# Optimization experiments

Measured on AMD Instinct MI355X. Metric: run time of the kernel, lower is better.

The kernel has to match this reference:

```python
import jax, jax.numpy as jnp
import numpy as np

IN, OUT, RANK = 4096, 4096, 8
ALPHA = 8.0

def _quantize_int8(x):
    # row-wise symmetric int8 quantization (matches torch _quantize_int8)
    scale = jnp.max(jnp.abs(x), axis=1) / 127.0              # [rows]
    q = jnp.round(x / jnp.clip(scale, 1e-12)[:, None]).astype(jnp.int8)
    return q, scale


def setup_inputs() -> dict:
    key = jax.random.key(0)
    k_x, k_w, k_a, k_b = jax.random.split(key, 4)
    x = jax.random.normal(k_x, (8192, IN), dtype=jnp.float32)
    # simulate quantizing a pretrained fp32 weight [OUT, IN]
    w = jax.random.normal(k_w, (OUT, IN), dtype=jnp.float32) * 0.02
    w_scale = jnp.max(jnp.abs(w), axis=1) / 127.0
    weight_i8 = jnp.round(w / jnp.clip(w_scale, 1e-12)[:, None]).astype(jnp.int8)
    weight_scale = w_scale.astype(jnp.float32)               # [OUT]
    # LoRA params (lora_b random instead of zeros so output is nontrivial)
    lora_a = jax.random.normal(k_a, (RANK, IN), dtype=jnp.float32) * (1.0 / np.sqrt(IN))
    lora_b = jax.random.normal(k_b, (OUT, RANK), dtype=jnp.float32) * 0.02
    return {"x": x, "weight_i8": weight_i8, "weight_scale": weight_scale,
            "lora_a": lora_a, "lora_b": lora_b}


def reference(x, weight_i8, weight_scale, lora_a, lora_b):
    # quantize_act=True path: int8 activation quant + int8 GEMM (int32 accum) + dequant
    x_i8, x_scale = _quantize_int8(x)                         # [T, IN] int8, [T]
    out_i32 = jnp.matmul(x_i8, weight_i8.T, preferred_element_type=jnp.int32)  # [T, OUT]
    out = out_i32.astype(jnp.float32) * x_scale[:, None] * weight_scale[None, :]
    # LoRA low-rank add: x @ A^T @ B^T * (alpha / rank)
    out = out + (x @ lora_a.T) @ lora_b.T * (ALPHA / RANK)
    return out
```

## Files before the change

kernel.cpp:

```cpp
#include <hip/hip_runtime.h>
#include <stdint.h>

#define T_DIM   8192
#define IN_DIM  4096
#define OUT_DIM 4096
#define RANK    8

typedef int v4i __attribute__((ext_vector_type(4)));

__device__ __forceinline__ void async_copy16(const void* g, void* l) {
  __builtin_amdgcn_global_load_lds(
      (const __attribute__((address_space(1))) void*)g,
      (__attribute__((address_space(3))) void*)l, 16, 0, 0);
}

#define PW_BLOCKS 16384
#define QX_BLOCKS 8192
#define LA_BLOCKS 16
#define XZ_BLOCKS 64
#define PREP_BLOCKS (PW_BLOCKS + QX_BLOCKS + LA_BLOCKS + XZ_BLOCKS)

__global__ __launch_bounds__(256) void prep(
    const int* __restrict__ w32,
    const float* __restrict__ x,
    const float* __restrict__ lora_a,
    int8_t* __restrict__ w8,
    int8_t* __restrict__ x_i8,
    float* __restrict__ x_scale,
    int8_t* __restrict__ a_i8,
    float* __restrict__ a_scale,
    float* __restrict__ xa)
{
  const int b = blockIdx.x;
  const int tid = threadIdx.x;
  __shared__ float red[4];

  if (b < PW_BLOCKS) {
    const int idx = b * 256 + tid;
    const int4 v = ((const int4*)w32)[idx];
    char4 q;
    q.x = (signed char)v.x; q.y = (signed char)v.y;
    q.z = (signed char)v.z; q.w = (signed char)v.w;
    ((char4*)w8)[idx] = q;
    return;
  }
  if (b < PW_BLOCKS + QX_BLOCKS) {
    const int row = b - PW_BLOCKS;
    const float4* xr = (const float4*)(x + (size_t)row * IN_DIM);
    float4 xv[4];
#pragma unroll
    for (int c = 0; c < 4; ++c) xv[c] = xr[c * 256 + tid];
    float am = 0.f;
#pragma unroll
    for (int c = 0; c < 4; ++c)
      am = fmaxf(am, fmaxf(fmaxf(fabsf(xv[c].x), fabsf(xv[c].y)),
                           fmaxf(fabsf(xv[c].z), fabsf(xv[c].w))));
#pragma unroll
    for (int off = 32; off > 0; off >>= 1)
      am = fmaxf(am, __shfl_xor(am, off, 64));
    if ((tid & 63) == 0) red[tid >> 6] = am;
    __syncthreads();
    const float amax = fmaxf(fmaxf(red[0], red[1]), fmaxf(red[2], red[3]));
    const float scale = amax * (1.0f / 127.0f);
    const float inv = 1.0f / fmaxf(scale, 1e-12f);
    char4* qout = (char4*)(x_i8 + (size_t)row * IN_DIM);
#pragma unroll
    for (int c = 0; c < 4; ++c) {
      char4 q;
      q.x = (signed char)(int)rintf(xv[c].x * inv);
      q.y = (signed char)(int)rintf(xv[c].y * inv);
      q.z = (signed char)(int)rintf(xv[c].z * inv);
      q.w = (signed char)(int)rintf(xv[c].w * inv);
      qout[c * 256 + tid] = q;
    }
    if (tid == 0) x_scale[row] = scale;
    return;
  }
  if (b < PW_BLOCKS + QX_BLOCKS + LA_BLOCKS) {
    const int r = b - (PW_BLOCKS + QX_BLOCKS);
    if (r >= RANK) {
      ((int4*)(a_i8 + (size_t)r * IN_DIM))[tid] = int4{0, 0, 0, 0};
      if (tid == 0) a_scale[r] = 0.f;
      return;
    }
    const float4* ar = (const float4*)(lora_a + (size_t)r * IN_DIM);
    float4 av[4];
#pragma unroll
    for (int c = 0; c < 4; ++c) av[c] = ar[c * 256 + tid];
    float am = 0.f;
#pragma unroll
    for (int c = 0; c < 4; ++c)
      am = fmaxf(am, fmaxf(fmaxf(fabsf(av[c].x), fabsf(av[c].y)),
                           fmaxf(fabsf(av[c].z), fabsf(av[c].w))));
#pragma unroll
    for (int off = 32; off > 0; off >>= 1)
      am = fmaxf(am, __shfl_xor(am, off, 64));
    if ((tid & 63) == 0) red[tid >> 6] = am;
    __syncthreads();
    const float amax = fmaxf(fmaxf(red[0], red[1]), fmaxf(red[2], red[3]));
    const float scale = amax * (1.0f / 127.0f);
    const float inv = 1.0f / fmaxf(scale, 1e-12f);
    char4* qout = (char4*)(a_i8 + (size_t)r * IN_DIM);
#pragma unroll
    for (int c = 0; c < 4; ++c) {
      char4 q;
      q.x = (signed char)(int)rintf(av[c].x * inv);
      q.y = (signed char)(int)rintf(av[c].y * inv);
      q.z = (signed char)(int)rintf(av[c].z * inv);
      q.w = (signed char)(int)rintf(av[c].w * inv);
      qout[c * 256 + tid] = q;
    }
    if (tid == 0) a_scale[r] = scale;
    return;
  }
  const int idx = (b - (PW_BLOCKS + QX_BLOCKS + LA_BLOCKS)) * 256 + tid;
  ((float4*)xa)[idx] = float4{0.f, 0.f, 0.f, 0.f};
}

__global__ __launch_bounds__(256) void xa_i8(
    const int8_t* __restrict__ x_i8, const float* __restrict__ x_scale,
    const int8_t* __restrict__ a_i8, const float* __restrict__ a_scale,
    float* __restrict__ xa)
{
  const int tid = threadIdx.x;
  const int lane = tid & 63, wave = tid >> 6;
  const int kb = blockIdx.x & 7;
  const int rb = blockIdx.x >> 3;
  const int m16 = lane & 15, quad = lane >> 4;
  const int row0 = rb * 64 + wave * 16;
  const int kbase = kb * 512;

  v4i acc = {0, 0, 0, 0};
  const int8_t* ap = x_i8 + (size_t)(row0 + m16) * IN_DIM + kbase + quad * 16;
  const int8_t* bp = a_i8 + (size_t)m16 * IN_DIM + kbase + quad * 16;
#pragma unroll
  for (int k = 0; k < 512; k += 64)
    acc = __builtin_amdgcn_mfma_i32_16x16x64_i8(
        *(const v4i*)(ap + k), *(const v4i*)(bp + k), acc, 0, 0, 0);

  if (m16 < RANK) {
    const float asc = a_scale[m16];
    const int r = row0 + quad * 4;
#pragma unroll
    for (int reg = 0; reg < 4; ++reg)
      atomicAdd(&xa[(size_t)(r + reg) * RANK + m16],
                (float)acc[reg] * x_scale[r + reg] * asc);
  }
}

__global__ __launch_bounds__(256) void int8_gemm_lora(
    const int8_t* __restrict__ A,
    const int8_t* __restrict__ B,
    const float* __restrict__ x_scale,
    const float* __restrict__ w_scale,
    const float* __restrict__ xa,
    const float* __restrict__ lora_b,
    float* __restrict__ out)
{
  __shared__ __align__(16) int8_t As[128 * 64];
  __shared__ __align__(16) int8_t Bs[128 * 64];
  __shared__ float xs_s[128];
  __shared__ float ws_s[128];
  __shared__ __align__(16) float xa_s[128 * RANK];
  __shared__ __align__(16) float lb_s[128 * RANK];

  const int tid = threadIdx.x;
  const int bx = blockIdx.x & 31;
  const int by = blockIdx.x >> 5;
  const size_t arow0 = (size_t)by * 128;
  const size_t brow0 = (size_t)bx * 128;

  if (tid < 128) xs_s[tid] = x_scale[arow0 + tid];
  else           ws_s[tid - 128] = w_scale[brow0 + (tid - 128)];
  ((float4*)xa_s)[tid] = ((const float4*)(xa + arow0 * RANK))[tid];
  ((float4*)lb_s)[tid] = ((const float4*)(lora_b + brow0 * RANK))[tid];

  v4i acc[4][4];
  const v4i vzero = {0, 0, 0, 0};
#pragma unroll
  for (int i = 0; i < 4; ++i)
#pragma unroll
    for (int j = 0; j < 4; ++j) acc[i][j] = vzero;

  const int lane = tid & 63;
  const int wave = tid >> 6;
  const int wr = wave >> 1, wc = wave & 1;
  const int quad = lane >> 4, m16 = lane & 15;

  const int8_t* a_frag_base = As + ((wr * 64 + m16) * 64 + quad * 16);
  const int8_t* b_frag_base = Bs + ((wc * 64 + m16) * 64 + quad * 16);

  const int off0 = tid * 16;
  const int r0 = tid >> 2;
  const int c0 = (tid & 3) * 16;
  const int8_t* a_src = A + (arow0 + (size_t)r0) * IN_DIM + c0;
  const int8_t* b_src = B + (brow0 + (size_t)r0) * IN_DIM + c0;

  for (int k0 = 0; k0 < IN_DIM; k0 += 64) {
    async_copy16(a_src + k0,                       As + off0);
    async_copy16(a_src + (size_t)64 * IN_DIM + k0, As + 4096 + off0);
    async_copy16(b_src + k0,                       Bs + off0);
    async_copy16(b_src + (size_t)64 * IN_DIM + k0, Bs + 4096 + off0);
    __syncthreads();

    v4i aF[4], bF[4];
#pragma unroll
    for (int i = 0; i < 4; ++i) aF[i] = *(const v4i*)(a_frag_base + i * 16 * 64);
#pragma unroll
    for (int j = 0; j < 4; ++j) bF[j] = *(const v4i*)(b_frag_base + j * 16 * 64);
#pragma unroll
    for (int i = 0; i < 4; ++i)
#pragma unroll
      for (int j = 0; j < 4; ++j)
        acc[i][j] = __builtin_amdgcn_mfma_i32_16x16x64_i8(aF[i], bF[j], acc[i][j], 0, 0, 0);
    __syncthreads();
  }

  float wscv[4];
  float4 lb0[4], lb1[4];
  int cols[4];
#pragma unroll
  for (int j = 0; j < 4; ++j) {
    const int c = wc * 64 + j * 16 + m16;
    cols[j] = c;
    wscv[j] = ws_s[c];
    lb0[j] = *(const float4*)(lb_s + c * RANK);
    lb1[j] = *(const float4*)(lb_s + c * RANK + 4);
  }
#pragma unroll
  for (int i = 0; i < 4; ++i) {
#pragma unroll
    for (int reg = 0; reg < 4; ++reg) {
      const int r = wr * 64 + i * 16 + quad * 4 + reg;
      const float xsc = xs_s[r];
      const float4 xa0 = *(const float4*)(xa_s + r * RANK);
      const float4 xa1 = *(const float4*)(xa_s + r * RANK + 4);
      float* orow = out + (arow0 + (size_t)r) * OUT_DIM + brow0;
#pragma unroll
      for (int j = 0; j < 4; ++j) {
        float v = (float)acc[i][j][reg] * xsc * wscv[j];
        v += xa0.x * lb0[j].x + xa0.y * lb0[j].y + xa0.z * lb0[j].z + xa0.w * lb0[j].w +
             xa1.x * lb1[j].x + xa1.y * lb1[j].y + xa1.z * lb1[j].z + xa1.w * lb1[j].w;
        orow[cols[j]] = v;
      }
    }
  }
}

extern "C" void kernel_launch(void* const* d_in, const int* in_sizes, int n_in,
                              void* d_out, int out_size, void* d_ws, size_t ws_size,
                              hipStream_t stream) {
  const float* x       = (const float*)d_in[0];
  const int*   w_i32   = (const int*)d_in[1];
  const float* w_scale = (const float*)d_in[2];
  const float* lora_a  = (const float*)d_in[3];
  const float* lora_b  = (const float*)d_in[4];
  float* out = (float*)d_out;

  int8_t* x_i8   = (int8_t*)d_ws;
  int8_t* w8     = x_i8 + (size_t)T_DIM * IN_DIM;
  int8_t* a_i8   = w8 + (size_t)OUT_DIM * IN_DIM;
  float*  a_scale = (float*)(a_i8 + (size_t)16 * IN_DIM);
  float*  x_scale = a_scale + 16;
  float*  xa      = x_scale + T_DIM;

  prep<<<PREP_BLOCKS, 256, 0, stream>>>(w_i32, x, lora_a, w8, x_i8, x_scale,
                                        a_i8, a_scale, xa);
  xa_i8<<<(T_DIM / 64) * 8, 256, 0, stream>>>(x_i8, x_scale, a_i8, a_scale, xa);
  int8_gemm_lora<<<(T_DIM / 128) * (OUT_DIM / 128), 256, 0, stream>>>(
      x_i8, w8, x_scale, w_scale, xa, lora_b, out);
}
```

Before: 451.9 us.

## Fuse LoRA x@A into quant prep and use 256x256 triple-buffered int8 GEMM

The LoRA x@A^T product is now computed in fp32 inside the activation-quantization blocks, reusing the loaded x row. This removes the separate lora_a quantization, the xa zeroing, the MFMA xa kernel and its atomics. The main GEMM moves to 256x256 tiles with 512 threads and a three-stage global_load_lds pipeline. It adds an XOR-swizzled LDS layout, a remapped block order for L2 locality, and setprio around the MFMAs. The larger tile raises register pressure (8x4 accumulators) and uses 96KB of LDS, which limits occupancy.

```diff
diff --git a/kernel.cpp b/kernel.cpp
--- a/kernel.cpp
+++ b/kernel.cpp
@@ -16,9 +16,7 @@
 
 #define PW_BLOCKS 16384
 #define QX_BLOCKS 8192
-#define LA_BLOCKS 16
-#define XZ_BLOCKS 64
-#define PREP_BLOCKS (PW_BLOCKS + QX_BLOCKS + LA_BLOCKS + XZ_BLOCKS)
+#define PREP_BLOCKS (PW_BLOCKS + QX_BLOCKS)
 
 __global__ __launch_bounds__(256) void prep(
     const int* __restrict__ w32,
@@ -27,13 +25,12 @@
     int8_t* __restrict__ w8,
     int8_t* __restrict__ x_i8,
     float* __restrict__ x_scale,
-    int8_t* __restrict__ a_i8,
-    float* __restrict__ a_scale,
     float* __restrict__ xa)
 {
   const int b = blockIdx.x;
   const int tid = threadIdx.x;
   __shared__ float red[4];
+  __shared__ float redx[4][RANK];
 
   if (b < PW_BLOCKS) {
     const int idx = b * 256 + tid;
@@ -44,111 +41,99 @@
     ((char4*)w8)[idx] = q;
     return;
   }
-  if (b < PW_BLOCKS + QX_BLOCKS) {
-    const int row = b - PW_BLOCKS;
-    const float4* xr = (const float4*)(x + (size_t)row * IN_DIM);
-    float4 xv[4];
-#pragma unroll
-    for (int c = 0; c < 4; ++c) xv[c] = xr[c * 256 + tid];
-    float am = 0.f;
-#pragma unroll
-    for (int c = 0; c < 4; ++c)
-      am = fmaxf(am, fmaxf(fmaxf(fabsf(xv[c].x), fabsf(xv[c].y)),
-                           fmaxf(fabsf(xv[c].z), fabsf(xv[c].w))));
-#pragma unroll
-    for (int off = 32; off > 0; off >>= 1)
-      am = fmaxf(am, __shfl_xor(am, off, 64));
-    if ((tid & 63) == 0) red[tid >> 6] = am;
-    __syncthreads();
-    const float amax = fmaxf(fmaxf(red[0], red[1]), fmaxf(red[2], red[3]));
-    const float scale = amax * (1.0f / 127.0f);
-    const float inv = 1.0f / fmaxf(scale, 1e-12f);
-    char4* qout = (char4*)(x_i8 + (size_t)row * IN_DIM);
+
+  const int row = b - PW_BLOCKS;
+  const float4* xr = (const float4*)(x + (size_t)row * IN_DIM);
+  float4 xv[4];
+#pragma unroll
+  for (int c = 0; c < 4; ++c) xv[c] = xr[c * 256 + tid];
+
+  float am = 0.f;
+#pragma unroll
+  for (int c = 0; c < 4; ++c)
+    am = fmaxf(am, fmaxf(fmaxf(fabsf(xv[c].x), fabsf(xv[c].y)),
+                         fmaxf(fabsf(xv[c].z), fabsf(xv[c].w))));
+#pragma unroll
+  for (int off = 32; off > 0; off >>= 1)
+    am = fmaxf(am, __shfl_xor(am, off, 64));
+  if ((tid & 63) == 0) red[tid >> 6] = am;
+
+  float dot[RANK];
+#pragma unroll
+  for (int r = 0; r < RANK; ++r) {
+    const float4* ar = (const float4*)(lora_a + (size_t)r * IN_DIM);
+    float s = 0.f;
 #pragma unroll
     for (int c = 0; c < 4; ++c) {
-      char4 q;
-      q.x = (signed char)(int)rintf(xv[c].x * inv);
-      q.y = (signed char)(int)rintf(xv[c].y * inv);
-      q.z = (signed char)(int)rintf(xv[c].z * inv);
-      q.w = (signed char)(int)rintf(xv[c].w * inv);
-      qout[c * 256 + tid] = q;
+      const float4 a = ar[c * 256 + tid];
+      s += xv[c].x * a.x + xv[c].y * a.y + xv[c].z * a.z + xv[c].w * a.w;
     }
-    if (tid == 0) x_scale[row] = scale;
-    return;
-  }
-  if (b < PW_BLOCKS + QX_BLOCKS + LA_BLOCKS) {
-    const int r = b - (PW_BLOCKS + QX_BLOCKS);
-    if (r >= RANK) {
-      ((int4*)(a_i8 + (size_t)r * IN_DIM))[tid] = int4{0, 0, 0, 0};
-      if (tid == 0) a_scale[r] = 0.f;
-      return;
-    }
-    const float4* ar = (const float4*)(lora_a + (size_t)r * IN_DIM);
-    float4 av[4];
-#pragma unroll
-    for (int c = 0; c < 4; ++c) av[c] = ar[c * 256 + tid];
-    float am = 0.f;
-#pragma unroll
-    for (int c = 0; c < 4; ++c)
-      am = fmaxf(am, fmaxf(fmaxf(fabsf(av[c].x), fabsf(av[c].y)),
-                           fmaxf(fabsf(av[c].z), fabsf(av[c].w))));
-#pragma unroll
-    for (int off = 32; off > 0; off >>= 1)
-      am = fmaxf(am, __shfl_xor(am, off, 64));
-    if ((tid & 63) == 0) red[tid >> 6] = am;
-    __syncthreads();
-    const float amax = fmaxf(fmaxf(red[0], red[1]), fmaxf(red[2], red[3]));
-    const float scale = amax * (1.0f / 127.0f);
-    const float inv = 1.0f / fmaxf(scale, 1e-12f);
-    char4* qout = (char4*)(a_i8 + (size_t)r * IN_DIM);
-#pragma unroll
-    for (int c = 0; c < 4; ++c) {
-      char4 q;
-      q.x = (signed char)(int)rintf(av[c].x * inv);
-      q.y = (signed char)(int)rintf(av[c].y * inv);
-      q.z = (signed char)(int)rintf(av[c].z * inv);
-      q.w = (signed char)(int)rintf(av[c].w * inv);
-      qout[c * 256 + tid] = q;
-    }
-    if (tid == 0) a_scale[r] = scale;
-    return;
-  }
-  const int idx = (b - (PW_BLOCKS + QX_BLOCKS + LA_BLOCKS)) * 256 + tid;
-  ((float4*)xa)[idx] = float4{0.f, 0.f, 0.f, 0.f};
-}
-
-__global__ __launch_bounds__(256) void xa_i8(
-    const int8_t* __restrict__ x_i8, const float* __restrict__ x_scale,
-    const int8_t* __restrict__ a_i8, const float* __restrict__ a_scale,
-    float* __restrict__ xa)
-{
-  const int tid = threadIdx.x;
-  const int lane = tid & 63, wave = tid >> 6;
-  const int kb = blockIdx.x & 7;
-  const int rb = blockIdx.x >> 3;
-  const int m16 = lane & 15, quad = lane >> 4;
-  const int row0 = rb * 64 + wave * 16;
-  const int kbase = kb * 512;
-
-  v4i acc = {0, 0, 0, 0};
-  const int8_t* ap = x_i8 + (size_t)(row0 + m16) * IN_DIM + kbase + quad * 16;
-  const int8_t* bp = a_i8 + (size_t)m16 * IN_DIM + kbase + quad * 16;
-#pragma unroll
-  for (int k = 0; k < 512; k += 64)
-    acc = __builtin_amdgcn_mfma_i32_16x16x64_i8(
-        *(const v4i*)(ap + k), *(const v4i*)(bp + k), acc, 0, 0, 0);
-
-  if (m16 < RANK) {
-    const float asc = a_scale[m16];
-    const int r = row0 + quad * 4;
-#pragma unroll
-    for (int reg = 0; reg < 4; ++reg)
-      atomicAdd(&xa[(size_t)(r + reg) * RANK + m16],
-                (float)acc[reg] * x_scale[r + reg] * asc);
-  }
-}
-
-__global__ __launch_bounds__(256) void int8_gemm_lora(
+    dot[r] = s;
+  }
+#pragma unroll
+  for (int off = 32; off > 0; off >>= 1) {
+#pragma unroll
+    for (int r = 0; r < RANK; ++r)
+      dot[r] += __shfl_xor(dot[r], off, 64);
+  }
+  if ((tid & 63) == 0) {
+#pragma unroll
+    for (int r = 0; r < RANK; ++r) redx[tid >> 6][r] = dot[r];
+  }
+  __syncthreads();
+
+  const float amax = fmaxf(fmaxf(red[0], red[1]), fmaxf(red[2], red[3]));
+  const float scale = amax * (1.0f / 127.0f);
+  const float inv = 1.0f / fmaxf(scale, 1e-12f);
+  char4* qout = (char4*)(x_i8 + (size_t)row * IN_DIM);
+#pragma unroll
+  for (int c = 0; c < 4; ++c) {
+    char4 q;
+    q.x = (signed char)(int)rintf(xv[c].x * inv);
+    q.y = (signed char)(int)rintf(xv[c].y * inv);
+    q.z = (signed char)(int)rintf(xv[c].z * inv);
+    q.w = (signed char)(int)rintf(xv[c].w * inv);
+    qout[c * 256 + tid] = q;
+  }
+  if (tid == 0) x_scale[row] = scale;
+  if (tid < RANK)
+    xa[(size_t)row * RANK + tid] =
+        redx[0][tid] + redx[1][tid] + redx[2][tid] + redx[3][tid];
+}
+
+#define SYNC(n) do {                                      \
+    asm volatile("s_waitcnt vmcnt(" #n ")" ::: "memory"); \
+    __builtin_amdgcn_s_barrier();                         \
+    __builtin_amdgcn_sched_barrier(0);                    \
+  } while (0)
+
+__device__ __forceinline__ void stage_tile(const int8_t* aSrc, const int8_t* bSrc,
+                                           int8_t* Lbuf, int ldsOff) {
+  async_copy16(aSrc,                          Lbuf + ldsOff);
+  async_copy16(aSrc + (size_t)128 * IN_DIM,   Lbuf + 8192 + ldsOff);
+  async_copy16(bSrc,                          Lbuf + 16384 + ldsOff);
+  async_copy16(bSrc + (size_t)128 * IN_DIM,   Lbuf + 16384 + 8192 + ldsOff);
+}
+
+__device__ __forceinline__ void compute_tile(const int8_t* Lbuf, int aOff, int bOff,
+                                             v4i (&acc)[8][4]) {
+  const int8_t* La = Lbuf;
+  const int8_t* Lb = Lbuf + 16384;
+  v4i aF[8], bF[4];
+#pragma unroll
+  for (int i = 0; i < 8; ++i) aF[i] = *(const v4i*)(La + aOff + i * 1024);
+#pragma unroll
+  for (int j = 0; j < 4; ++j) bF[j] = *(const v4i*)(Lb + bOff + j * 1024);
+  __builtin_amdgcn_s_setprio(1);
+#pragma unroll
+  for (int i = 0; i < 8; ++i)
+#pragma unroll
+    for (int j = 0; j < 4; ++j)
+      acc[i][j] = __builtin_amdgcn_mfma_i32_16x16x64_i8(aF[i], bF[j], acc[i][j], 0, 0, 0);
+  __builtin_amdgcn_s_setprio(0);
+}
+
+__global__ __launch_bounds__(512, 2) void gemm256_i8(
     const int8_t* __restrict__ A,
     const int8_t* __restrict__ B,
     const float* __restrict__ x_scale,
@@ -157,64 +142,76 @@
     const float* __restrict__ lora_b,
     float* __restrict__ out)
 {
-  __shared__ __align__(16) int8_t As[128 * 64];
-  __shared__ __align__(16) int8_t Bs[128 * 64];
-  __shared__ float xs_s[128];
-  __shared__ float ws_s[128];
-  __shared__ __align__(16) float xa_s[128 * RANK];
-  __shared__ __align__(16) float lb_s[128 * RANK];
-
+  __shared__ __align__(16) int8_t smem[3 * 32768];
   const int tid = threadIdx.x;
-  const int bx = blockIdx.x & 31;
-  const int by = blockIdx.x >> 5;
-  const size_t arow0 = (size_t)by * 128;
-  const size_t brow0 = (size_t)bx * 128;
-
-  if (tid < 128) xs_s[tid] = x_scale[arow0 + tid];
-  else           ws_s[tid - 128] = w_scale[brow0 + (tid - 128)];
+
+  const int orig = blockIdx.x;
+  const int wgid = ((orig & 7) << 6) | (orig >> 3);
+  const int by = wgid >> 4;
+  const int bx = wgid & 15;
+  const size_t arow0 = (size_t)by * 256;
+  const size_t brow0 = (size_t)bx * 256;
+
+  const int r_l = tid >> 2;
+  const int qsw = ((tid & 3) ^ ((r_l >> 1) & 3)) << 4;
+  const int8_t* aSrc = A + (arow0 + r_l) * IN_DIM + qsw;
+  const int8_t* bSrc = B + (brow0 + r_l) * IN_DIM + qsw;
+  const int ldsOff = tid << 4;
+
+  const int lane = tid & 63;
+  const int wave = tid >> 6;
+  const int wr = wave >> 2, wc = wave & 3;
+  const int m16 = lane & 15, quad = lane >> 4;
+  const int sw = (quad ^ ((m16 >> 1) & 3)) << 4;
+  const int aOff = (wr * 128 + m16) * 64 + sw;
+  const int bOff = (wc * 64 + m16) * 64 + sw;
+
+  v4i acc[8][4];
+  const v4i vz = {0, 0, 0, 0};
+#pragma unroll
+  for (int i = 0; i < 8; ++i)
+#pragma unroll
+    for (int j = 0; j < 4; ++j) acc[i][j] = vz;
+
+  stage_tile(aSrc, bSrc, smem, ldsOff);
+  stage_tile(aSrc + 64, bSrc + 64, smem + 32768, ldsOff);
+
+#pragma unroll 1
+  for (int t = 0; t < 60; t += 3) {
+    SYNC(4);
+    stage_tile(aSrc + (t + 2) * 64, bSrc + (t + 2) * 64, smem + 2 * 32768, ldsOff);
+    compute_tile(smem, aOff, bOff, acc);
+    SYNC(4);
+    stage_tile(aSrc + (t + 3) * 64, bSrc + (t + 3) * 64, smem, ldsOff);
+    compute_tile(smem + 32768, aOff, bOff, acc);
+    SYNC(4);
+    stage_tile(aSrc + (t + 4) * 64, bSrc + (t + 4) * 64, smem + 32768, ldsOff);
+    compute_tile(smem + 2 * 32768, aOff, bOff, acc);
+  }
+  SYNC(4);
+  stage_tile(aSrc + 62 * 64, bSrc + 62 * 64, smem + 2 * 32768, ldsOff);
+  compute_tile(smem, aOff, bOff, acc);
+  SYNC(4);
+  stage_tile(aSrc + 63 * 64, bSrc + 63 * 64, smem, ldsOff);
+  compute_tile(smem + 32768, aOff, bOff, acc);
+  SYNC(4);
+  compute_tile(smem + 2 * 32768, aOff, bOff, acc);
+  asm volatile("s_waitcnt vmcnt(0)" ::: "memory");
+  __builtin_amdgcn_s_barrier();
+  __builtin_amdgcn_sched_barrier(0);
+  compute_tile(smem, aOff, bOff, acc);
+
+  __syncthreads();
+  float* fs   = (float*)smem;
+  float* xs_s = fs;
+  float* ws_s = fs + 256;
+  float* xa_s = fs + 512;
+  float* lb_s = fs + 2560;
+  if (tid < 256) xs_s[tid] = x_scale[arow0 + tid];
+  else           ws_s[tid - 256] = w_scale[brow0 + (tid - 256)];
   ((float4*)xa_s)[tid] = ((const float4*)(xa + arow0 * RANK))[tid];
   ((float4*)lb_s)[tid] = ((const float4*)(lora_b + brow0 * RANK))[tid];
-
-  v4i acc[4][4];
-  const v4i vzero = {0, 0, 0, 0};
-#pragma unroll
-  for (int i = 0; i < 4; ++i)
-#pragma unroll
-    for (int j = 0; j < 4; ++j) acc[i][j] = vzero;
-
-  const int lane = tid & 63;
-  const int wave = tid >> 6;
-  const int wr = wave >> 1, wc = wave & 1;
-  const int quad = lane >> 4, m16 = lane & 15;
-
-  const int8_t* a_frag_base = As + ((wr * 64 + m16) * 64 + quad * 16);
-  const int8_t* b_frag_base = Bs + ((wc * 64 + m16) * 64 + quad * 16);
-
-  const int off0 = tid * 16;
-  const int r0 = tid >> 2;
-  const int c0 = (tid & 3) * 16;
-  const int8_t* a_src = A + (arow0 + (size_t)r0) * IN_DIM + c0;
-  const int8_t* b_src = B + (brow0 + (size_t)r0) * IN_DIM + c0;
-
-  for (int k0 = 0; k0 < IN_DIM; k0 += 64) {
-    async_copy16(a_src + k0,                       As + off0);
-    async_copy16(a_src + (size_t)64 * IN_DIM + k0, As + 4096 + off0);
-    async_copy16(b_src + k0,                       Bs + off0);
-    async_copy16(b_src + (size_t)64 * IN_DIM + k0, Bs + 4096 + off0);
-    __syncthreads();
-
-    v4i aF[4], bF[4];
-#pragma unroll
-    for (int i = 0; i < 4; ++i) aF[i] = *(const v4i*)(a_frag_base + i * 16 * 64);
-#pragma unroll
-    for (int j = 0; j < 4; ++j) bF[j] = *(const v4i*)(b_frag_base + j * 16 * 64);
-#pragma unroll
-    for (int i = 0; i < 4; ++i)
-#pragma unroll
-      for (int j = 0; j < 4; ++j)
-        acc[i][j] = __builtin_amdgcn_mfma_i32_16x16x64_i8(aF[i], bF[j], acc[i][j], 0, 0, 0);
-    __syncthreads();
-  }
+  __syncthreads();
 
   float wscv[4];
   float4 lb0[4], lb1[4];
@@ -228,10 +225,10 @@
     lb1[j] = *(const float4*)(lb_s + c * RANK + 4);
   }
 #pragma unroll
-  for (int i = 0; i < 4; ++i) {
+  for (int i = 0; i < 8; ++i) {
 #pragma unroll
     for (int reg = 0; reg < 4; ++reg) {
-      const int r = wr * 64 + i * 16 + quad * 4 + reg;
+      const int r = wr * 128 + i * 16 + quad * 4 + reg;
       const float xsc = xs_s[r];
       const float4 xa0 = *(const float4*)(xa_s + r * RANK);
       const float4 xa1 = *(const float4*)(xa_s + r * RANK + 4);
@@ -257,16 +254,12 @@
   const float* lora_b  = (const float*)d_in[4];
   float* out = (float*)d_out;
 
-  int8_t* x_i8   = (int8_t*)d_ws;
-  int8_t* w8     = x_i8 + (size_t)T_DIM * IN_DIM;
-  int8_t* a_i8   = w8 + (size_t)OUT_DIM * IN_DIM;
-  float*  a_scale = (float*)(a_i8 + (size_t)16 * IN_DIM);
-  float*  x_scale = a_scale + 16;
+  int8_t* x_i8    = (int8_t*)d_ws;
+  int8_t* w8      = x_i8 + (size_t)T_DIM * IN_DIM;
+  float*  x_scale = (float*)(w8 + (size_t)OUT_DIM * IN_DIM);
   float*  xa      = x_scale + T_DIM;
 
-  prep<<<PREP_BLOCKS, 256, 0, stream>>>(w_i32, x, lora_a, w8, x_i8, x_scale,
-                                        a_i8, a_scale, xa);
-  xa_i8<<<(T_DIM / 64) * 8, 256, 0, stream>>>(x_i8, x_scale, a_i8, a_scale, xa);
-  int8_gemm_lora<<<(T_DIM / 128) * (OUT_DIM / 128), 256, 0, stream>>>(
+  prep<<<PREP_BLOCKS, 256, 0, stream>>>(w_i32, x, lora_a, w8, x_i8, x_scale, xa);
+  gemm256_i8<<<(T_DIM / 256) * (OUT_DIM / 256), 512, 0, stream>>>(
       x_i8, w8, x_scale, w_scale, xa, lora_b, out);
 }
```

New measurement: 407.9 us. 1.11x faster.
